# Kernel tuning notes

Measured on AMD Instinct MI355X. Metric: run time of the kernel, lower is better.

The kernel has to match this reference:

```python
import jax, jax.numpy as jnp
import numpy as np

N_EMBD = 1024
N_HEAD = 16
HEAD_DIM = N_EMBD // N_HEAD


def setup_inputs() -> dict:
    key = jax.random.key(0)
    kx, kqkv, kw, kb = jax.random.split(key, 4)
    B, T = 4, 2048
    x = jax.random.normal(kx, (B, T, N_EMBD), dtype=jnp.float32)
    # nn.Linear weights stored [out, in]; apply as x @ W.T
    w_qkv = jax.random.normal(kqkv, (3 * N_EMBD, N_EMBD), dtype=jnp.float32) * (N_EMBD ** -0.5)
    w_out = jax.random.normal(kw, (N_EMBD, N_EMBD), dtype=jnp.float32) * (N_EMBD ** -0.5)
    b_out = jax.random.normal(kb, (N_EMBD,), dtype=jnp.float32) * 0.01
    return {"x": x, "w_qkv": w_qkv, "w_out": w_out, "b_out": b_out}


def reference(x, w_qkv, w_out, b_out):
    B, T, C = x.shape
    H, D = N_HEAD, HEAD_DIM
    qkv = jnp.einsum('btc,fc->btf', x, w_qkv)  # [B,T,3C]
    q, k, v = jnp.split(qkv, 3, axis=-1)
    q = q.reshape(B, T, H, D).transpose(0, 2, 1, 3)  # [B,H,T,D]
    k = k.reshape(B, T, H, D).transpose(0, 2, 1, 3)
    v = v.reshape(B, T, H, D).transpose(0, 2, 1, 3)
    att = jnp.einsum('bhqd,bhkd->bhqk', q, k) * (D ** -0.5)  # [B,H,T,T]
    causal = jnp.tril(jnp.ones((T, T), dtype=bool))
    att = jnp.where(causal[None, None], att, jnp.float32(-jnp.inf))
    att = jax.nn.softmax(att, axis=-1)
    out = jnp.einsum('bhqk,bhkd->bhqd', att, v)  # [B,H,T,D]
    out = out.transpose(0, 2, 1, 3).reshape(B, T, C)
    return jnp.einsum('btc,oc->bto', out, w_out) + b_out
```

## Files before the change

kernel.cpp:

```cpp
#include <hip/hip_runtime.h>
#include <stdint.h>

#define SEQ 2048
#define C3 3072
#define C1 1024

typedef __bf16 bf16x8 __attribute__((ext_vector_type(8)));
typedef short short8 __attribute__((ext_vector_type(8)));
typedef float f32x4 __attribute__((ext_vector_type(4)));
typedef float f32x16 __attribute__((ext_vector_type(16)));
typedef unsigned uintx2 __attribute__((ext_vector_type(2)));
typedef const __attribute__((address_space(1))) void gv_t;
typedef __attribute__((address_space(3))) void lv_t;

#if __has_builtin(__builtin_amdgcn_exp2f)
#define EXP2(x) __builtin_amdgcn_exp2f(x)
#else
#define EXP2(x) exp2f(x)
#endif

static __device__ __forceinline__ unsigned short f2bf(float f) {
  union { float ff; unsigned u; } x; x.ff = f;
  unsigned u = x.u + 0x7FFFu + ((x.u >> 16) & 1u);
  return (unsigned short)(u >> 16);
}
static __device__ __forceinline__ unsigned rne2(float lo, float hi) {
  return (unsigned)f2bf(lo) | ((unsigned)f2bf(hi) << 16);
}
static __device__ __forceinline__ unsigned pk2(float lo, float hi) {
  union { float f; unsigned u; } a, b; a.f = lo; b.f = hi;
  return __builtin_amdgcn_perm(b.u, a.u, 0x07060302);
}

static __device__ __forceinline__ void plswap(unsigned a, unsigned b,
                                              unsigned& o0, unsigned& o1) {
#if __has_builtin(__builtin_amdgcn_permlane32_swap)
  uintx2 r = __builtin_amdgcn_permlane32_swap(a, b, false, false);
  o0 = r[0]; o1 = r[1];
#else
  asm volatile("v_permlane32_swap_b32 %0, %1" : "+v"(a), "+v"(b));
  o0 = a; o1 = b;
#endif
}

__global__ void k_cvt3(const float* __restrict__ ia, const float* __restrict__ ib,
                       const float* __restrict__ ic, unsigned short* __restrict__ oa,
                       unsigned short* __restrict__ ob, unsigned short* __restrict__ oc) {
  int blk = blockIdx.x;
  const float* in; unsigned short* out; int base;
  if (blk < 8192)      { in = ia; out = oa; base = blk; }
  else if (blk < 11264){ in = ib; out = ob; base = blk - 8192; }
  else                 { in = ic; out = oc; base = blk - 11264; }
  int i = base * 256 + threadIdx.x;
  f32x4 v = ((const f32x4*)in)[i];
  ushort4 o;
  o.x = f2bf(v[0]); o.y = f2bf(v[1]); o.z = f2bf(v[2]); o.w = f2bf(v[3]);
  ((ushort4*)out)[i] = o;
}

template<int MODE>
__global__ __launch_bounds__(256, 3) void k_gemm(
    const unsigned short* __restrict__ A, const unsigned short* __restrict__ B,
    void* __restrict__ Cout, const float* __restrict__ bias,
    unsigned short* __restrict__ vTout, int M, int N, int K)
{
  __shared__ unsigned short As[128 * 64];
  __shared__ unsigned short Bs[128 * 64];
  const int tid = threadIdx.x;
  const int w = tid >> 6, l = tid & 63;
  const int lane15 = l & 15, quad = l >> 4;
  const int m0 = blockIdx.y * 128, n0 = blockIdx.x * 128;
  const int wm = (w >> 1) * 64, wn = (w & 1) * 64;

  f32x4 acc[4][4];
#pragma unroll
  for (int i = 0; i < 4; i++)
#pragma unroll
    for (int j = 0; j < 4; j++) acc[i][j] = (f32x4){0.f, 0.f, 0.f, 0.f};

  const int srow = l >> 3;
  const int g_off = ((l & 7) ^ (srow & 7)) * 8;
  const unsigned short* Ab = A + (size_t)(m0 + w * 32 + srow) * K + g_off;
  const unsigned short* Bb = B + (size_t)(n0 + w * 32 + srow) * K + g_off;
  const int rsl = lane15 & 7;

  for (int k0 = 0; k0 < K; k0 += 64) {
    __syncthreads();
#pragma unroll
    for (int i = 0; i < 4; i++) {
      int rb = w * 32 + i * 8;
      __builtin_amdgcn_global_load_lds((gv_t*)(Ab + (size_t)(i * 8) * K + k0),
                                       (lv_t*)&As[rb * 64], 16, 0, 0);
      __builtin_amdgcn_global_load_lds((gv_t*)(Bb + (size_t)(i * 8) * K + k0),
                                       (lv_t*)&Bs[rb * 64], 16, 0, 0);
    }
    __syncthreads();
#pragma unroll
    for (int s = 0; s < 2; s++) {
      bf16x8 af[4], bfr[4];
      const int slot = ((s * 4 + quad) ^ rsl) * 8;
#pragma unroll
      for (int t = 0; t < 4; t++) {
        af[t]  = *(const bf16x8*)&As[(wm + t * 16 + lane15) * 64 + slot];
        bfr[t] = *(const bf16x8*)&Bs[(wn + t * 16 + lane15) * 64 + slot];
      }
#pragma unroll
      for (int i = 0; i < 4; i++)
#pragma unroll
        for (int j = 0; j < 4; j++)
          acc[i][j] = __builtin_amdgcn_mfma_f32_16x16x32_bf16(af[i], bfr[j], acc[i][j], 0, 0, 0);
    }
  }

  if (MODE == 0) {
    if (n0 >= 2048) {
#pragma unroll
      for (int i = 0; i < 4; i++) {
        int rowb = m0 + wm + i * 16 + quad * 4;
        int bb = rowb >> 11, t = rowb & 2047;
#pragma unroll
        for (int j = 0; j < 4; j++) {
          int hd = n0 + wn + j * 16 + lane15 - 2048;
          unsigned short* vp = vTout +
              ((size_t)((bb << 4) + (hd >> 6)) * 64 + (hd & 63)) * SEQ + t;
          *(uint2*)vp = make_uint2(rne2(acc[i][j][0], acc[i][j][1]),
                                   rne2(acc[i][j][2], acc[i][j][3]));
        }
      }
    } else {
      unsigned short* Cp = (unsigned short*)Cout;
      const float s = (n0 < 1024) ? 0.18033688f : 1.0f;
#pragma unroll
      for (int i = 0; i < 4; i++) {
        int rowb = m0 + wm + i * 16 + quad * 4;
#pragma unroll
        for (int j = 0; j < 4; j++) {
          int col = n0 + wn + j * 16 + lane15;
#pragma unroll
          for (int r = 0; r < 4; r++)
            Cp[(size_t)(rowb + r) * N + col] = f2bf(acc[i][j][r] * s);
        }
      }
    }
  } else {
    float* Cp = (float*)Cout;
#pragma unroll
    for (int i = 0; i < 4; i++) {
      int rowb = m0 + wm + i * 16 + quad * 4;
#pragma unroll
      for (int j = 0; j < 4; j++) {
        int col = n0 + wn + j * 16 + lane15;
        float bv = bias[col];
#pragma unroll
        for (int r = 0; r < 4; r++)
          Cp[(size_t)(rowb + r) * N + col] = acc[i][j][r] + bv;
      }
    }
  }
}


static __device__ __forceinline__ void stage_kv(
    unsigned short* bufp, const unsigned short* __restrict__ qkv,
    const unsigned short* __restrict__ vT, size_t tokb, int bh, int h,
    int k0, int w, int krow_l, int kslot, int vrow_l, int vslot)
{
  unsigned short* Kb = bufp;
  unsigned short* Vb = bufp + 8192;
#pragma unroll
  for (int i = 0; i < 4; i++) {
    int rb = (w * 4 + i) * 8;
    int row = rb + krow_l;
    int ck = kslot ^ (row & 7);
    const unsigned short* g = qkv + (tokb + k0 + row) * C3 + C1 + h * 64 + ck * 8;
    __builtin_amdgcn_global_load_lds((gv_t*)g, (lv_t*)&Kb[rb * 64], 16, 0, 0);
  }
#pragma unroll
  for (int i = 0; i < 4; i++) {
    int rb = (w * 4 + i) * 4;
    int row = rb + vrow_l;
    int ck = vslot ^ (row & 15);
    const unsigned short* g = vT + ((size_t)bh * 64 + row) * SEQ + k0 + ck * 8;
    __builtin_amdgcn_global_load_lds((gv_t*)g, (lv_t*)&Vb[rb * 128], 16, 0, 0);
  }
}

static __device__ __forceinline__ void attn_tile(
    f32x16* O, float& lrun, const bf16x8* qf,
    const unsigned short* Kb, const unsigned short* Vb,
    bool diag, int k0, int qmy, int w, int l31, int hl)
{
#pragma unroll
  for (int ht = 0; ht < 2; ht++) {
    if (diag && (ht * 2 > w)) continue;
    const bool two = !diag || (ht * 2 + 1 <= w);

#pragma unroll
    for (int lm = 0; lm < 2; lm++) {
      if (lm == 1 && !two) continue;
      const int mt = ht * 2 + lm;

      f32x16 stL;
#pragma unroll
      for (int i = 0; i < 16; i++) stL[i] = -16.f;
      {
        int row = mt * 32 + l31;
        const unsigned short* kr = &Kb[row * 64];
        __builtin_amdgcn_s_setprio(1);
#pragma unroll
        for (int ks = 0; ks < 4; ks++) {
          bf16x8 a = *(const bf16x8*)&kr[((((ks << 1) | hl)) ^ (row & 7)) * 8];
          stL = __builtin_amdgcn_mfma_f32_32x32x16_bf16(a, qf[ks], stL, 0, 0, 0);
        }
        __builtin_amdgcn_s_setprio(0);
      }

      if (diag && mt == w) {
#pragma unroll
        for (int r = 0; r < 16; r++) {
          int key = k0 + w * 32 + (r & 3) + ((r >> 2) << 3) + (hl << 2);
          if (key > qmy) stL[r] = -1e30f;
        }
      }

      float ps0 = 0.f, ps1 = 0.f, ps2 = 0.f, ps3 = 0.f;
      unsigned pk[8];
#pragma unroll
      for (int r = 0; r < 16; r += 4) {
        float p0 = EXP2(stL[r]);
        float p1 = EXP2(stL[r + 1]);
        float p2 = EXP2(stL[r + 2]);
        float p3 = EXP2(stL[r + 3]);
        ps0 += p0; ps1 += p1; ps2 += p2; ps3 += p3;
        pk[(r >> 1)]     = pk2(p0, p1);
        pk[(r >> 1) + 1] = pk2(p2, p3);
      }
      lrun += (ps0 + ps1) + (ps2 + ps3);

      bf16x8 vf[2][2];
#pragma unroll
      for (int e = 0; e < 2; e++) {
        int kk = ht * 4 + lm * 2 + e;
#pragma unroll
        for (int dt = 0; dt < 2; dt++) {
          int row = dt * 32 + l31;
          vf[e][dt] = *(const bf16x8*)&Vb[row * 128 + (((2 * kk + hl)) ^ (row & 15)) * 8];
        }
      }

#pragma unroll
      for (int e = 0; e < 2; e++) {
        union { unsigned u[4]; bf16x8 v; } Bf;
        plswap(pk[4 * e],     pk[4 * e + 2], Bf.u[0], Bf.u[2]);
        plswap(pk[4 * e + 1], pk[4 * e + 3], Bf.u[1], Bf.u[3]);
        __builtin_amdgcn_s_setprio(1);
        O[0] = __builtin_amdgcn_mfma_f32_32x32x16_bf16(vf[e][0], Bf.v, O[0], 0, 0, 0);
        O[1] = __builtin_amdgcn_mfma_f32_32x32x16_bf16(vf[e][1], Bf.v, O[1], 0, 0, 0);
        __builtin_amdgcn_s_setprio(0);
      }
    }
  }
}

static __device__ __forceinline__ void attn_epi(
    const f32x16* O, float lrun, unsigned short* buf,
    unsigned short* __restrict__ att, size_t tokb, int q0, int h,
    int w, int l, int l31, int hl)
{
  lrun += __shfl_xor(lrun, 32, 64);
  float linv = __builtin_amdgcn_rcpf(lrun);
  unsigned* epi32 = (unsigned*)buf;
  const int base = w * 2304 + l31 * 72;
  __builtin_amdgcn_s_waitcnt(0);
#pragma unroll
  for (int dt = 0; dt < 2; dt++)
#pragma unroll
    for (int c = 0; c < 4; c++) {
      int d0 = dt * 32 + c * 8 + hl * 4;
      epi32[(base + d0) >> 1]     = rne2(O[dt][4 * c] * linv, O[dt][4 * c + 1] * linv);
      epi32[(base + d0 + 2) >> 1] = rne2(O[dt][4 * c + 2] * linv, O[dt][4 * c + 3] * linv);
    }
  __builtin_amdgcn_s_waitcnt(0);
  {
    int q = l >> 1, hf = l & 1;
    const unsigned short* ep = &buf[w * 2304 + q * 72 + hf * 32];
    unsigned short* og = att + (tokb + q0 + w * 32 + q) * C1 + h * 64 + hf * 32;
#pragma unroll
    for (int c2 = 0; c2 < 4; c2++)
      *(bf16x8*)(og + c2 * 8) = *(const bf16x8*)&ep[c2 * 8];
  }
}

__global__ __launch_bounds__(256, 2) void k_attn(
    const unsigned short* __restrict__ qkv, const unsigned short* __restrict__ vT,
    unsigned short* __restrict__ att)
{
  __shared__ unsigned short buf[2][16384];
  const int tid = threadIdx.x;
  const int w = tid >> 6, l = tid & 63;
  const int l31 = l & 31, hl = l >> 5;
  const int bh = blockIdx.x, b = bh >> 4, h = bh & 15;
  const int yq = blockIdx.y;
  const int qt_lo = yq, qt_hi = 15 - yq;
  const int q0l = qt_lo << 7, q0h = qt_hi << 7;
  const int nkt = qt_hi + 1;
  const size_t tokb = (size_t)b * SEQ;
  const int qmy_l = q0l + w * 32 + l31;
  const int qmy_h = q0h + w * 32 + l31;

  const int krow_l = l >> 3, kslot = l & 7;
  const int vrow_l = l >> 4, vslot = l & 15;

  bf16x8 qfh[4], qfl[4];
  {
    const unsigned short* qph = qkv + (tokb + q0h + w * 32 + l31) * C3 + h * 64 + hl * 8;
    const unsigned short* qpl = qkv + (tokb + q0l + w * 32 + l31) * C3 + h * 64 + hl * 8;
#pragma unroll
    for (int ks = 0; ks < 4; ks++) {
      qfh[ks] = *(const bf16x8*)(qph + ks * 16);
      qfl[ks] = *(const bf16x8*)(qpl + ks * 16);
    }
  }

  f32x16 Oh[2], Ol[2];
#pragma unroll
  for (int i = 0; i < 16; i++) { Oh[0][i] = 0.f; Oh[1][i] = 0.f; Ol[0][i] = 0.f; Ol[1][i] = 0.f; }
  float lrh = 0.f, lrl = 0.f;

  stage_kv(&buf[0][0], qkv, vT, tokb, bh, h, 0, w, krow_l, kslot, vrow_l, vslot);

  int cur = 0;
  for (int kt = 0; kt < nkt; kt++) {
    asm volatile("s_waitcnt vmcnt(0)" ::: "memory");
    __builtin_amdgcn_s_barrier();
    if (kt + 1 < nkt)
      stage_kv(&buf[cur ^ 1][0], qkv, vT, tokb, bh, h, (kt + 1) << 7,
               w, krow_l, kslot, vrow_l, vslot);

    const unsigned short* Kb = &buf[cur][0];
    const unsigned short* Vb = &buf[cur][8192];
    const int k0 = kt << 7;

    attn_tile(Oh, lrh, qfh, Kb, Vb, kt == qt_hi, k0, qmy_h, w, l31, hl);
    if (kt <= qt_lo)
      attn_tile(Ol, lrl, qfl, Kb, Vb, kt == qt_lo, k0, qmy_l, w, l31, hl);

    cur ^= 1;
  }

  __syncthreads();
  attn_epi(Oh, lrh, &buf[0][0], att, tokb, q0h, h, w, l, l31, hl);
  attn_epi(Ol, lrl, &buf[0][0], att, tokb, q0l, h, w, l, l31, hl);
}

extern "C" void kernel_launch(void* const* d_in, const int* in_sizes, int n_in,
                              void* d_out, int out_size, void* d_ws, size_t ws_size,
                              hipStream_t stream) {
  const float* x     = (const float*)d_in[0];
  const float* w_qkv = (const float*)d_in[1];
  const float* w_out = (const float*)d_in[2];
  const float* b_out = (const float*)d_in[3];
  float* out = (float*)d_out;

  unsigned short* xb  = (unsigned short*)d_ws;
  unsigned short* wqb = xb  + (size_t)8192 * 1024;
  unsigned short* wob = wqb + (size_t)3072 * 1024;
  unsigned short* qkv = wob + (size_t)1024 * 1024;
  unsigned short* att = qkv + (size_t)8192 * 3072;
  unsigned short* vT  = att + (size_t)8192 * 1024;

  k_cvt3<<<12288, 256, 0, stream>>>(x, w_qkv, w_out, xb, wqb, wob);
  k_gemm<0><<<dim3(24, 64), 256, 0, stream>>>(xb, wqb, (void*)qkv, nullptr, vT, 8192, 3072, 1024);
  k_attn<<<dim3(64, 8), 256, 0, stream>>>(qkv, vT, att);
  k_gemm<1><<<dim3(8, 64), 256, 0, stream>>>(att, wob, (void*)out, b_out, nullptr, 8192, 1024, 1024);
}
```

Baseline: 221.8 us.

## Double-buffer GEMM with 8-wave 128x256 tiles and split prefetch; batch cvt work

The GEMM kernel now runs 512 threads (8 waves) on 128x256 output tiles with double-buffered LDS. The next K-tile's global-to-LDS loads are issued in two parts, interleaved with the MFMA phases, and synchronised through explicit vmcnt waits and raw barriers. s_setprio is raised around the MFMA bursts. The conversion kernel handles four vectors per thread and launches a quarter as many blocks. The aim is to hide load latency and cut the number of barriers per K-step, at the cost of more LDS per block, lower occupancy, and fewer blocks for the output projection (256 blocks).

Result: slower. 243.7 us (+9.9%).

```diff
diff --git a/kernel.cpp b/kernel.cpp
--- a/kernel.cpp
+++ b/kernel.cpp
@@ -43,34 +43,42 @@
 #endif
 }
 
+#define GLD(src, dst) __builtin_amdgcn_global_load_lds((gv_t*)(src), (lv_t*)(dst), 16, 0, 0)
+
 __global__ void k_cvt3(const float* __restrict__ ia, const float* __restrict__ ib,
                        const float* __restrict__ ic, unsigned short* __restrict__ oa,
                        unsigned short* __restrict__ ob, unsigned short* __restrict__ oc) {
   int blk = blockIdx.x;
   const float* in; unsigned short* out; int base;
-  if (blk < 8192)      { in = ia; out = oa; base = blk; }
-  else if (blk < 11264){ in = ib; out = ob; base = blk - 8192; }
-  else                 { in = ic; out = oc; base = blk - 11264; }
-  int i = base * 256 + threadIdx.x;
-  f32x4 v = ((const f32x4*)in)[i];
-  ushort4 o;
-  o.x = f2bf(v[0]); o.y = f2bf(v[1]); o.z = f2bf(v[2]); o.w = f2bf(v[3]);
-  ((ushort4*)out)[i] = o;
+  if (blk < 2048)     { in = ia; out = oa; base = blk; }
+  else if (blk < 2816){ in = ib; out = ob; base = blk - 2048; }
+  else                { in = ic; out = oc; base = blk - 2816; }
+  int i0 = base * 1024 + threadIdx.x;
+#pragma unroll
+  for (int j = 0; j < 4; j++) {
+    int i = i0 + j * 256;
+    f32x4 v = ((const f32x4*)in)[i];
+    ushort4 o;
+    o.x = f2bf(v[0]); o.y = f2bf(v[1]); o.z = f2bf(v[2]); o.w = f2bf(v[3]);
+    ((ushort4*)out)[i] = o;
+  }
 }
 
 template<int MODE>
-__global__ __launch_bounds__(256, 3) void k_gemm(
+__global__ __launch_bounds__(512, 2) void k_gemm8(
     const unsigned short* __restrict__ A, const unsigned short* __restrict__ B,
     void* __restrict__ Cout, const float* __restrict__ bias,
     unsigned short* __restrict__ vTout, int M, int N, int K)
 {
-  __shared__ unsigned short As[128 * 64];
-  __shared__ unsigned short Bs[128 * 64];
+  __shared__ unsigned short As[2 * 128 * 64];
+  __shared__ unsigned short Bs[2 * 256 * 64];
   const int tid = threadIdx.x;
   const int w = tid >> 6, l = tid & 63;
-  const int lane15 = l & 15, quad = l >> 4;
-  const int m0 = blockIdx.y * 128, n0 = blockIdx.x * 128;
-  const int wm = (w >> 1) * 64, wn = (w & 1) * 64;
+  const int wr = w >> 2, wc = w & 3;
+  const int lane15 = l & 15, quad = l >> 4, rsl = lane15 & 7;
+  const int m0 = blockIdx.y * 128, n0 = blockIdx.x * 256;
+  const int srow = l >> 3, sslot = l & 7;
+  const int nt = K >> 6;
 
   f32x4 acc[4][4];
 #pragma unroll
@@ -78,82 +86,127 @@
 #pragma unroll
     for (int j = 0; j < 4; j++) acc[i][j] = (f32x4){0.f, 0.f, 0.f, 0.f};
 
-  const int srow = l >> 3;
-  const int g_off = ((l & 7) ^ (srow & 7)) * 8;
-  const unsigned short* Ab = A + (size_t)(m0 + w * 32 + srow) * K + g_off;
-  const unsigned short* Bb = B + (size_t)(n0 + w * 32 + srow) * K + g_off;
-  const int rsl = lane15 & 7;
-
-  for (int k0 = 0; k0 < K; k0 += 64) {
-    __syncthreads();
-#pragma unroll
-    for (int i = 0; i < 4; i++) {
-      int rb = w * 32 + i * 8;
-      __builtin_amdgcn_global_load_lds((gv_t*)(Ab + (size_t)(i * 8) * K + k0),
-                                       (lv_t*)&As[rb * 64], 16, 0, 0);
-      __builtin_amdgcn_global_load_lds((gv_t*)(Bb + (size_t)(i * 8) * K + k0),
-                                       (lv_t*)&Bs[rb * 64], 16, 0, 0);
-    }
-    __syncthreads();
-#pragma unroll
-    for (int s = 0; s < 2; s++) {
-      bf16x8 af[4], bfr[4];
-      const int slot = ((s * 4 + quad) ^ rsl) * 8;
-#pragma unroll
-      for (int t = 0; t < 4; t++) {
-        af[t]  = *(const bf16x8*)&As[(wm + t * 16 + lane15) * 64 + slot];
-        bfr[t] = *(const bf16x8*)&Bs[(wn + t * 16 + lane15) * 64 + slot];
-      }
-#pragma unroll
-      for (int i = 0; i < 4; i++)
-#pragma unroll
-        for (int j = 0; j < 4; j++)
-          acc[i][j] = __builtin_amdgcn_mfma_f32_16x16x32_bf16(af[i], bfr[j], acc[i][j], 0, 0, 0);
-    }
+  const int ckoff = (sslot ^ srow) * 8;
+  const int jb0 = 2 * w, jb1 = 2 * w + 1;
+  const int rbB[2][2] = {
+    { (jb0 >> 2) * 64 + (jb0 & 3) * 8,      (jb1 >> 2) * 64 + (jb1 & 3) * 8 },
+    { (jb0 >> 2) * 64 + 32 + (jb0 & 3) * 8, (jb1 >> 2) * 64 + 32 + (jb1 & 3) * 8 } };
+
+  GLD(A + (size_t)(m0 + w * 16 + srow) * K + ckoff,            &As[w * 1024]);
+  GLD(A + (size_t)(m0 + w * 16 + 8 + srow) * K + ckoff,        &As[w * 1024 + 512]);
+  GLD(B + (size_t)(n0 + rbB[0][0] + srow) * K + ckoff,         &Bs[rbB[0][0] * 64]);
+  GLD(B + (size_t)(n0 + rbB[0][1] + srow) * K + ckoff,         &Bs[rbB[0][1] * 64]);
+  GLD(B + (size_t)(n0 + rbB[1][0] + srow) * K + ckoff,         &Bs[rbB[1][0] * 64]);
+  GLD(B + (size_t)(n0 + rbB[1][1] + srow) * K + ckoff,         &Bs[rbB[1][1] * 64]);
+  asm volatile("s_waitcnt vmcnt(2)" ::: "memory");
+  __builtin_amdgcn_s_barrier();
+
+  int cur = 0;
+  for (int t = 0; t < nt; ++t) {
+    const int k1 = (t + 1) << 6;
+    const bool more = (t + 1 < nt);
+    const unsigned cA = cur * 8192, cB = cur * 16384;
+    const unsigned dA = (cur ^ 1) * 8192, dB = (cur ^ 1) * 16384;
+
+    bf16x8 af[4][2], bfr[2][2];
+#pragma unroll
+    for (int fm = 0; fm < 4; fm++)
+#pragma unroll
+      for (int kk = 0; kk < 2; kk++)
+        af[fm][kk] = *(const bf16x8*)&As[cA + (wr * 64 + fm * 16 + lane15) * 64 +
+                                         (((kk << 2) | quad) ^ rsl) * 8];
+#pragma unroll
+    for (int f2 = 0; f2 < 2; f2++)
+#pragma unroll
+      for (int kk = 0; kk < 2; kk++)
+        bfr[f2][kk] = *(const bf16x8*)&Bs[cB + (wc * 64 + f2 * 16 + lane15) * 64 +
+                                          (((kk << 2) | quad) ^ rsl) * 8];
+    if (more) {
+      GLD(A + (size_t)(m0 + w * 16 + srow) * K + k1 + ckoff,     &As[dA + w * 1024]);
+      GLD(A + (size_t)(m0 + w * 16 + 8 + srow) * K + k1 + ckoff, &As[dA + w * 1024 + 512]);
+      GLD(B + (size_t)(n0 + rbB[0][0] + srow) * K + k1 + ckoff,  &Bs[dB + rbB[0][0] * 64]);
+      asm volatile("s_waitcnt vmcnt(3)" ::: "memory");
+    } else {
+      asm volatile("s_waitcnt vmcnt(0)" ::: "memory");
+    }
+    __builtin_amdgcn_s_barrier();
+    __builtin_amdgcn_s_setprio(1);
+#pragma unroll
+    for (int kk = 0; kk < 2; kk++)
+#pragma unroll
+      for (int fm = 0; fm < 4; fm++) {
+        acc[fm][0] = __builtin_amdgcn_mfma_f32_16x16x32_bf16(af[fm][kk], bfr[0][kk], acc[fm][0], 0, 0, 0);
+        acc[fm][1] = __builtin_amdgcn_mfma_f32_16x16x32_bf16(af[fm][kk], bfr[1][kk], acc[fm][1], 0, 0, 0);
+      }
+    __builtin_amdgcn_s_setprio(0);
+
+#pragma unroll
+    for (int f2 = 0; f2 < 2; f2++)
+#pragma unroll
+      for (int kk = 0; kk < 2; kk++)
+        bfr[f2][kk] = *(const bf16x8*)&Bs[cB + (wc * 64 + (2 + f2) * 16 + lane15) * 64 +
+                                          (((kk << 2) | quad) ^ rsl) * 8];
+    if (more) {
+      GLD(B + (size_t)(n0 + rbB[0][1] + srow) * K + k1 + ckoff, &Bs[dB + rbB[0][1] * 64]);
+      GLD(B + (size_t)(n0 + rbB[1][0] + srow) * K + k1 + ckoff, &Bs[dB + rbB[1][0] * 64]);
+      GLD(B + (size_t)(n0 + rbB[1][1] + srow) * K + k1 + ckoff, &Bs[dB + rbB[1][1] * 64]);
+    }
+    asm volatile("s_waitcnt vmcnt(2)" ::: "memory");
+    __builtin_amdgcn_s_barrier();
+    __builtin_amdgcn_s_setprio(1);
+#pragma unroll
+    for (int kk = 0; kk < 2; kk++)
+#pragma unroll
+      for (int fm = 0; fm < 4; fm++) {
+        acc[fm][2] = __builtin_amdgcn_mfma_f32_16x16x32_bf16(af[fm][kk], bfr[0][kk], acc[fm][2], 0, 0, 0);
+        acc[fm][3] = __builtin_amdgcn_mfma_f32_16x16x32_bf16(af[fm][kk], bfr[1][kk], acc[fm][3], 0, 0, 0);
+      }
+    __builtin_amdgcn_s_setprio(0);
+    cur ^= 1;
   }
 
   if (MODE == 0) {
     if (n0 >= 2048) {
 #pragma unroll
-      for (int i = 0; i < 4; i++) {
-        int rowb = m0 + wm + i * 16 + quad * 4;
-        int bb = rowb >> 11, t = rowb & 2047;
-#pragma unroll
-        for (int j = 0; j < 4; j++) {
-          int hd = n0 + wn + j * 16 + lane15 - 2048;
+      for (int fm = 0; fm < 4; fm++) {
+        int row = m0 + wr * 64 + fm * 16 + quad * 4;
+        int bb = row >> 11, tk = row & 2047;
+#pragma unroll
+        for (int fn = 0; fn < 4; fn++) {
+          int hd = n0 + wc * 64 + fn * 16 + lane15 - 2048;
           unsigned short* vp = vTout +
-              ((size_t)((bb << 4) + (hd >> 6)) * 64 + (hd & 63)) * SEQ + t;
-          *(uint2*)vp = make_uint2(rne2(acc[i][j][0], acc[i][j][1]),
-                                   rne2(acc[i][j][2], acc[i][j][3]));
+              ((size_t)((bb << 4) + (hd >> 6)) * 64 + (hd & 63)) * SEQ + tk;
+          *(uint2*)vp = make_uint2(rne2(acc[fm][fn][0], acc[fm][fn][1]),
+                                   rne2(acc[fm][fn][2], acc[fm][fn][3]));
         }
       }
     } else {
       unsigned short* Cp = (unsigned short*)Cout;
       const float s = (n0 < 1024) ? 0.18033688f : 1.0f;
 #pragma unroll
-      for (int i = 0; i < 4; i++) {
-        int rowb = m0 + wm + i * 16 + quad * 4;
-#pragma unroll
-        for (int j = 0; j < 4; j++) {
-          int col = n0 + wn + j * 16 + lane15;
+      for (int fm = 0; fm < 4; fm++) {
+        int row = m0 + wr * 64 + fm * 16 + quad * 4;
+#pragma unroll
+        for (int fn = 0; fn < 4; fn++) {
+          int col = n0 + wc * 64 + fn * 16 + lane15;
 #pragma unroll
           for (int r = 0; r < 4; r++)
-            Cp[(size_t)(rowb + r) * N + col] = f2bf(acc[i][j][r] * s);
+            Cp[(size_t)(row + r) * N + col] = f2bf(acc[fm][fn][r] * s);
         }
       }
     }
   } else {
     float* Cp = (float*)Cout;
 #pragma unroll
-    for (int i = 0; i < 4; i++) {
-      int rowb = m0 + wm + i * 16 + quad * 4;
-#pragma unroll
-      for (int j = 0; j < 4; j++) {
-        int col = n0 + wn + j * 16 + lane15;
+    for (int fm = 0; fm < 4; fm++) {
+      int row = m0 + wr * 64 + fm * 16 + quad * 4;
+#pragma unroll
+      for (int fn = 0; fn < 4; fn++) {
+        int col = n0 + wc * 64 + fn * 16 + lane15;
         float bv = bias[col];
 #pragma unroll
         for (int r = 0; r < 4; r++)
-          Cp[(size_t)(rowb + r) * N + col] = acc[i][j][r] + bv;
+          Cp[(size_t)(row + r) * N + col] = acc[fm][fn][r] + bv;
       }
     }
   }
@@ -173,7 +226,7 @@
     int row = rb + krow_l;
     int ck = kslot ^ (row & 7);
     const unsigned short* g = qkv + (tokb + k0 + row) * C3 + C1 + h * 64 + ck * 8;
-    __builtin_amdgcn_global_load_lds((gv_t*)g, (lv_t*)&Kb[rb * 64], 16, 0, 0);
+    GLD(g, &Kb[rb * 64]);
   }
 #pragma unroll
   for (int i = 0; i < 4; i++) {
@@ -181,7 +234,7 @@
     int row = rb + vrow_l;
     int ck = vslot ^ (row & 15);
     const unsigned short* g = vT + ((size_t)bh * 64 + row) * SEQ + k0 + ck * 8;
-    __builtin_amdgcn_global_load_lds((gv_t*)g, (lv_t*)&Vb[rb * 128], 16, 0, 0);
+    GLD(g, &Vb[rb * 128]);
   }
 }
 
@@ -369,8 +422,8 @@
   unsigned short* att = qkv + (size_t)8192 * 3072;
   unsigned short* vT  = att + (size_t)8192 * 1024;
 
-  k_cvt3<<<12288, 256, 0, stream>>>(x, w_qkv, w_out, xb, wqb, wob);
-  k_gemm<0><<<dim3(24, 64), 256, 0, stream>>>(xb, wqb, (void*)qkv, nullptr, vT, 8192, 3072, 1024);
+  k_cvt3<<<3072, 256, 0, stream>>>(x, w_qkv, w_out, xb, wqb, wob);
+  k_gemm8<0><<<dim3(12, 64), 512, 0, stream>>>(xb, wqb, (void*)qkv, nullptr, vT, 8192, 3072, 1024);
   k_attn<<<dim3(64, 8), 256, 0, stream>>>(qkv, vT, att);
-  k_gemm<1><<<dim3(8, 64), 256, 0, stream>>>(att, wob, (void*)out, b_out, nullptr, 8192, 1024, 1024);
-}
+  k_gemm8<1><<<dim3(4, 64), 512, 0, stream>>>(att, wob, (void*)out, b_out, nullptr, 8192, 1024, 1024);
+}
```
